# Kernel tuning notes

Measured on AMD Instinct MI355X. Metric: run time of the kernel, lower is better.

## Reference

```python
import jax, jax.numpy as jnp
import numpy as np

K, N = 1024, 16384


def setup_inputs() -> dict:
    key = jax.random.key(0)
    k0, k1, k2 = jax.random.split(key, 3)
    # event counts (non-negative), like the COVID case-count observations
    obs = jax.random.uniform(k0, (K, N), dtype=jnp.float32) * 10.0
    # Beta ~ U(1, 3), Alpha ~ U(0, 0.01) per the torch parameter init
    Beta = 1.0 + 2.0 * jax.random.uniform(k1, (K,), dtype=jnp.float32)
    Alpha = 0.01 * jax.random.uniform(k2, (K, K), dtype=jnp.float32)
    return {"obs": obs, "Beta": Beta, "Alpha": Alpha}


def reference(obs, Beta, Alpha):
    """Hawkes log-likelihood, exact O(N*K) recursion replacing the O(N^2*K^2) loop.

    Original per-step math (t > 0):
      lam1[k, t] = softplus( sum_j Alpha[k, j] * sum_{tp < t} obs[j, tp] * Beta[j] * exp(-(t - tp) * Beta[j]) )
    The exponential kernel gives S_{t+1} = exp(-Beta) * (S_t + obs[:, t]), S_0 = 0,
    where S_t[j] = sum_{tp < t} obs[j, tp] * exp(-(t - tp) * Beta[j]).
    lam1[:, 0] = 0 exactly (the torch code returns zeros at t = 0, not softplus(0)).
    """
    Mu0 = obs.mean(axis=1) / 10.0 + 1e-5                      # [K] background rate
    decay = jnp.exp(-Beta)                                    # [K]

    def step(S, o_t):                                         # S: [K], o_t: [K]
        return decay * (S + o_t), S                           # emit S_t, carry S_{t+1}

    _, S_seq = jax.lax.scan(step, jnp.zeros_like(Beta), obs.T)  # S_seq: [N, K]

    G = Beta[None, :] * S_seq                                 # [N, K] = Beta_j * S_t[j]
    lam1 = jax.nn.softplus(G @ Alpha.T).T                     # [K, N]; row k = softplus(Alpha @ g_t)
    lam1 = lam1.at[:, 0].set(0.0)                             # t = 0 branch returns zeros

    lams0 = jnp.broadcast_to(Mu0[:, None], obs.shape)         # [K, N]
    Nloglams = obs * jnp.log(lams0 + lam1 + 1e-5)
    loglik = (Nloglams - lams0 - lam1).sum()
    return loglik, lams0, lam1
```

## Files before the change

### kernel.cpp

```cpp
#include <hip/hip_runtime.h>
#include <hip/hip_bf16.h>
#include <stdint.h>

#define K_DIM 1024
#define N_DIM 16384

typedef __attribute__((ext_vector_type(8))) short short8;
typedef __attribute__((ext_vector_type(4))) float floatx4;

__device__ __forceinline__ void async_copy16(const void* g, void* l) {
  __builtin_amdgcn_global_load_lds((const __attribute__((address_space(1))) void*)g,
                                   (__attribute__((address_space(3))) void*)l,
                                   16, 0, 0);
}

__device__ __forceinline__ unsigned short f2bf(float x) {
  uint32_t u = __float_as_uint(x);
  u += 0x7fffu + ((u >> 16) & 1u);
  return (unsigned short)(u >> 16);
}

__global__ __launch_bounds__(256) void convert_alpha(const float* __restrict__ A,
                                                     unsigned short* __restrict__ Abf) {
  int idx = (blockIdx.x * 256 + threadIdx.x) * 4;
  floatx4 v = *(const floatx4*)(A + idx);
  ushort4 o;
  o.x = f2bf(v[0]); o.y = f2bf(v[1]); o.z = f2bf(v[2]); o.w = f2bf(v[3]);
  *(ushort4*)(Abf + idx) = o;
}

__global__ __launch_bounds__(256) void scan_kernel(const float* __restrict__ obs,
                                                   const float* __restrict__ Beta,
                                                   unsigned short* __restrict__ Gt,
                                                   float* __restrict__ mu_acc) {
  __shared__ float tile[64][177];
  const int tw = blockIdx.x;
  const int jg = blockIdx.y;
  const int j0 = jg * 64;
  const int t0 = tw * 128;
  const int tid = threadIdx.x;

  for (int u = tid; u < 64 * 44; u += 256) {
    int row = u / 44;
    int c4 = u % 44;
    int tloc = c4 * 4;
    int tg = t0 - 48 + tloc;
    float4 v;
    if (tg >= 0) {
      v = *(const float4*)(obs + (size_t)(j0 + row) * N_DIM + tg);
    } else {
      v = make_float4(0.f, 0.f, 0.f, 0.f);
    }
    tile[row][tloc]     = v.x;
    tile[row][tloc + 1] = v.y;
    tile[row][tloc + 2] = v.z;
    tile[row][tloc + 3] = v.w;
  }
  __syncthreads();

  {
    int row = tid & 63;
    int qq = tid >> 6;
    float s = 0.f;
    #pragma unroll 8
    for (int i = 0; i < 32; ++i) s += tile[row][48 + qq * 32 + i];
    atomicAdd(&mu_acc[j0 + row], s);
  }

  const int w = tid >> 6;
  const int lane = tid & 63;
  const int j = j0 + lane;
  const float beta = Beta[j];
  const float decay = expf(-beta);
  const int lt0 = w * 32;
  float S = 0.f;
  #pragma unroll
  for (int i = 0; i < 48; ++i) S = decay * (S + tile[lane][lt0 + i]);
  const int tg = t0 + w * 32;
  #pragma unroll
  for (int i = 0; i < 32; ++i) {
    Gt[(size_t)(tg + i) * K_DIM + j] = f2bf(beta * S);
    S = decay * (S + tile[lane][lt0 + 48 + i]);
  }
}

__global__ __launch_bounds__(256) void gemm_kernel(const unsigned short* __restrict__ A,
                                                   const unsigned short* __restrict__ B,
                                                   const float* __restrict__ obs,
                                                   const float* __restrict__ mu_acc,
                                                   float* __restrict__ lam1_out,
                                                   double* __restrict__ acc_out) {
  const int tb = blockIdx.x;
  const int kb = blockIdx.y;
  const int tid = threadIdx.x;
  const int lane = tid & 63, w = tid >> 6;
  const int wm = w >> 1, wn = w & 1;
  const int ml = lane & 15, q = lane >> 4;

  __shared__ unsigned short As[128 * 64];
  __shared__ unsigned short Bs[128 * 64];
  __shared__ float wsum[4];

  floatx4 acc[4][4] = {};

  const unsigned short* Ab = A + (size_t)kb * 128 * K_DIM;
  const unsigned short* Bb = B + (size_t)tb * 128 * K_DIM;

  for (int kt = 0; kt < 16; ++kt) {
    const unsigned short* Ak = Ab + kt * 64;
    const unsigned short* Bk = Bb + kt * 64;
    #pragma unroll
    for (int it = 0; it < 4; ++it) {
      int L = w * 256 + it * 64 + lane;
      int r = L >> 3;
      int c = L & 7;
      int cg = c ^ (r & 7);
      async_copy16(Ak + (size_t)r * K_DIM + cg * 8, &As[L * 8]);
      async_copy16(Bk + (size_t)r * K_DIM + cg * 8, &Bs[L * 8]);
    }
    __syncthreads();

    #pragma unroll
    for (int kk = 0; kk < 2; ++kk) {
      short8 a[4], b[4];
      #pragma unroll
      for (int mf = 0; mf < 4; ++mf) {
        int r = wm * 64 + mf * 16 + ml;
        int c = (kk * 4 + q) ^ (r & 7);
        a[mf] = *(const short8*)&As[r * 64 + c * 8];
      }
      #pragma unroll
      for (int nf = 0; nf < 4; ++nf) {
        int r = wn * 64 + nf * 16 + ml;
        int c = (kk * 4 + q) ^ (r & 7);
        b[nf] = *(const short8*)&Bs[r * 64 + c * 8];
      }
      #pragma unroll
      for (int mf = 0; mf < 4; ++mf)
        #pragma unroll
        for (int nf = 0; nf < 4; ++nf)
          acc[mf][nf] = __builtin_amdgcn_mfma_f32_16x16x32_bf16(a[mf], b[nf], acc[mf][nf], 0, 0, 0);
    }
    __syncthreads();
  }

  float lsum = 0.f;
  const int kblk = kb * 128 + wm * 64;
  const int tblk = tb * 128 + wn * 64;
  #pragma unroll
  for (int mf = 0; mf < 4; ++mf) {
    int k4 = kblk + mf * 16 + q * 4;
    floatx4 mu4 = *(const floatx4*)&mu_acc[k4];
    #pragma unroll
    for (int r = 0; r < 4; ++r) {
      int k = k4 + r;
      float mu = mu4[r] * (1.0f / 163840.0f) + 1e-5f;
      #pragma unroll
      for (int nf = 0; nf < 4; ++nf) {
        int t = tblk + nf * 16 + ml;
        float raw = acc[mf][nf][r];
        float lam = fmaxf(raw, 0.f) + log1pf(expf(-fabsf(raw)));
        if (t == 0) lam = 0.f;
        lam1_out[(size_t)k * N_DIM + t] = lam;
        float o = obs[(size_t)k * N_DIM + t];
        lsum += o * logf(mu + lam + 1e-5f) - mu - lam;
      }
    }
  }
  #pragma unroll
  for (int off = 32; off > 0; off >>= 1) lsum += __shfl_down(lsum, off);
  if (lane == 0) wsum[w] = lsum;
  __syncthreads();
  if (tid == 0) atomicAdd(acc_out, (double)(wsum[0] + wsum[1] + wsum[2] + wsum[3]));
}

__global__ __launch_bounds__(256) void finalize_kernel(const float* __restrict__ mu_acc,
                                                       const double* __restrict__ acc,
                                                       float* __restrict__ out) {
  int k = blockIdx.x;
  float mu = mu_acc[k] * (1.0f / 163840.0f) + 1e-5f;
  float* dst = out + 1 + (size_t)k * N_DIM;
  for (int t = threadIdx.x; t < N_DIM; t += 256) dst[t] = mu;
  if (blockIdx.x == 0 && threadIdx.x == 0) out[0] = (float)(*acc);
}

extern "C" void kernel_launch(void* const* d_in, const int* in_sizes, int n_in,
                              void* d_out, int out_size, void* d_ws, size_t ws_size,
                              hipStream_t stream) {
  const float* obs   = (const float*)d_in[0];
  const float* Beta  = (const float*)d_in[1];
  const float* Alpha = (const float*)d_in[2];
  float* out = (float*)d_out;

  double* acc  = (double*)d_ws;
  float* mu_acc = (float*)((char*)d_ws + 16);

  unsigned short* Gt  = (unsigned short*)(out + 4);
  unsigned short* Abf = Gt + (size_t)N_DIM * K_DIM;

  hipMemsetAsync(d_ws, 0, 16 + K_DIM * sizeof(float), stream);

  convert_alpha<<<dim3(K_DIM * K_DIM / (256 * 4)), 256, 0, stream>>>(Alpha, Abf);

  scan_kernel<<<dim3(N_DIM / 128, K_DIM / 64), 256, 0, stream>>>(obs, Beta, Gt, mu_acc);

  gemm_kernel<<<dim3(N_DIM / 128, K_DIM / 128), 256, 0, stream>>>(
      Abf, Gt, obs, mu_acc, out + 1 + (size_t)K_DIM * N_DIM, acc);

  finalize_kernel<<<dim3(K_DIM), 256, 0, stream>>>(mu_acc, acc, out);
}
```

Before: 329.7 us.

## Split row-mean into own kernel, shorten scan warmup, fast math, vectorize fill

Moves the per-row mean into a dedicated reduction kernel, which removes the atomics from the scan kernel. The scan warmup halo drops from 48 to 32 steps, so each block loads less data and does less recurrence work. The catch is that the history truncation gets looser: decay^32 with beta at least 1 is still tiny. The softplus and log in the GEMM epilogue now use fast intrinsics, and the finalize broadcast uses aligned float4 stores. The cost is an extra pass that reads all of obs once more.

```diff
diff --git a/kernel.cpp b/kernel.cpp
--- a/kernel.cpp
+++ b/kernel.cpp
@@ -29,22 +29,38 @@
   *(ushort4*)(Abf + idx) = o;
 }
 
+__global__ __launch_bounds__(256) void mu_kernel(const float* __restrict__ obs,
+                                                 float* __restrict__ mu_acc) {
+  const int k = blockIdx.x;
+  const float* row = obs + (size_t)k * N_DIM;
+  float s = 0.f;
+  for (int t = threadIdx.x * 4; t < N_DIM; t += 256 * 4) {
+    float4 v = *(const float4*)(row + t);
+    s += (v.x + v.y) + (v.z + v.w);
+  }
+  #pragma unroll
+  for (int off = 32; off > 0; off >>= 1) s += __shfl_down(s, off);
+  __shared__ float ws[4];
+  if ((threadIdx.x & 63) == 0) ws[threadIdx.x >> 6] = s;
+  __syncthreads();
+  if (threadIdx.x == 0) mu_acc[k] = (ws[0] + ws[1]) + (ws[2] + ws[3]);
+}
+
 __global__ __launch_bounds__(256) void scan_kernel(const float* __restrict__ obs,
                                                    const float* __restrict__ Beta,
-                                                   unsigned short* __restrict__ Gt,
-                                                   float* __restrict__ mu_acc) {
-  __shared__ float tile[64][177];
+                                                   unsigned short* __restrict__ Gt) {
+  __shared__ float tile[64][161];
   const int tw = blockIdx.x;
   const int jg = blockIdx.y;
   const int j0 = jg * 64;
   const int t0 = tw * 128;
   const int tid = threadIdx.x;
 
-  for (int u = tid; u < 64 * 44; u += 256) {
-    int row = u / 44;
-    int c4 = u % 44;
+  for (int u = tid; u < 64 * 40; u += 256) {
+    int row = u / 40;
+    int c4 = u % 40;
     int tloc = c4 * 4;
-    int tg = t0 - 48 + tloc;
+    int tg = t0 - 32 + tloc;
     float4 v;
     if (tg >= 0) {
       v = *(const float4*)(obs + (size_t)(j0 + row) * N_DIM + tg);
@@ -57,15 +73,6 @@
     tile[row][tloc + 3] = v.w;
   }
   __syncthreads();
-
-  {
-    int row = tid & 63;
-    int qq = tid >> 6;
-    float s = 0.f;
-    #pragma unroll 8
-    for (int i = 0; i < 32; ++i) s += tile[row][48 + qq * 32 + i];
-    atomicAdd(&mu_acc[j0 + row], s);
-  }
 
   const int w = tid >> 6;
   const int lane = tid & 63;
@@ -75,12 +82,12 @@
   const int lt0 = w * 32;
   float S = 0.f;
   #pragma unroll
-  for (int i = 0; i < 48; ++i) S = decay * (S + tile[lane][lt0 + i]);
+  for (int i = 0; i < 32; ++i) S = decay * (S + tile[lane][lt0 + i]);
   const int tg = t0 + w * 32;
   #pragma unroll
   for (int i = 0; i < 32; ++i) {
     Gt[(size_t)(tg + i) * K_DIM + j] = f2bf(beta * S);
-    S = decay * (S + tile[lane][lt0 + 48 + i]);
+    S = decay * (S + tile[lane][lt0 + 32 + i]);
   }
 }
 
@@ -159,11 +166,12 @@
       for (int nf = 0; nf < 4; ++nf) {
         int t = tblk + nf * 16 + ml;
         float raw = acc[mf][nf][r];
-        float lam = fmaxf(raw, 0.f) + log1pf(expf(-fabsf(raw)));
+        float e = __expf(-fabsf(raw));
+        float lam = fmaxf(raw, 0.f) + __logf(1.f + e);
         if (t == 0) lam = 0.f;
         lam1_out[(size_t)k * N_DIM + t] = lam;
         float o = obs[(size_t)k * N_DIM + t];
-        lsum += o * logf(mu + lam + 1e-5f) - mu - lam;
+        lsum += o * __logf(mu + lam + 1e-5f) - mu - lam;
       }
     }
   }
@@ -180,8 +188,12 @@
   int k = blockIdx.x;
   float mu = mu_acc[k] * (1.0f / 163840.0f) + 1e-5f;
   float* dst = out + 1 + (size_t)k * N_DIM;
-  for (int t = threadIdx.x; t < N_DIM; t += 256) dst[t] = mu;
-  if (blockIdx.x == 0 && threadIdx.x == 0) out[0] = (float)(*acc);
+  int tid = threadIdx.x;
+  if (tid < 3) dst[tid] = mu;
+  float4 v4 = make_float4(mu, mu, mu, mu);
+  for (int t = 3 + tid * 4; t + 3 < N_DIM; t += 256 * 4) *(float4*)(dst + t) = v4;
+  if (tid == 3) dst[N_DIM - 1] = mu;
+  if (blockIdx.x == 0 && tid == 4) out[0] = (float)(*acc);
 }
 
 extern "C" void kernel_launch(void* const* d_in, const int* in_sizes, int n_in,
@@ -192,17 +204,19 @@
   const float* Alpha = (const float*)d_in[2];
   float* out = (float*)d_out;
 
-  double* acc  = (double*)d_ws;
+  double* acc   = (double*)d_ws;
   float* mu_acc = (float*)((char*)d_ws + 16);
 
   unsigned short* Gt  = (unsigned short*)(out + 4);
   unsigned short* Abf = Gt + (size_t)N_DIM * K_DIM;
 
-  hipMemsetAsync(d_ws, 0, 16 + K_DIM * sizeof(float), stream);
+  hipMemsetAsync(d_ws, 0, 16, stream);
 
   convert_alpha<<<dim3(K_DIM * K_DIM / (256 * 4)), 256, 0, stream>>>(Alpha, Abf);
 
-  scan_kernel<<<dim3(N_DIM / 128, K_DIM / 64), 256, 0, stream>>>(obs, Beta, Gt, mu_acc);
+  mu_kernel<<<dim3(K_DIM), 256, 0, stream>>>(obs, mu_acc);
+
+  scan_kernel<<<dim3(N_DIM / 128, K_DIM / 64), 256, 0, stream>>>(obs, Beta, Gt);
 
   gemm_kernel<<<dim3(N_DIM / 128, K_DIM / 128), 256, 0, stream>>>(
       Abf, Gt, obs, mu_acc, out + 1 + (size_t)K_DIM * N_DIM, acc);
```

After: 294.7 us. 10.6% less time.
